# Kernel tuning notes

Hardware: AMD Instinct MI355X
Metric: run time of the kernel (lower is better)

Reference implementation:

```python
import jax, jax.numpy as jnp
import numpy as np
from jax import lax

H, W = 64, 64          # image_shape grid
TOP_K = 3
N_ITER = 50
EPS = 1e-8
NPTS = 3072            # N = M feature points (<= H*W)
SQRT2 = 1.4142135623730951
INV_SQRT3 = 1.0 / 1.7320508075688772


def setup_inputs() -> dict:
    key = jax.random.key(0)
    P = jax.random.uniform(key, (NPTS + 1, NPTS + 1), dtype=jnp.float32)
    K = jnp.array([[500.0, 0.0, 320.0],
                   [0.0, 500.0, 240.0],
                   [0.0, 0.0, 1.0]], dtype=jnp.float32)
    return {"P": P, "K": K}


def _power_iter(Mm, v0):
    # n_iter steps of v <- Mm @ v / ||.||  (differentiable via scan)
    def step(v, _):
        v = Mm @ v
        return v / (jnp.linalg.norm(v) + EPS), None
    v, _ = lax.scan(step, v0, None, length=N_ITER)
    return v


def _det3(M):
    return (M[0, 0] * (M[1, 1] * M[2, 2] - M[1, 2] * M[2, 1])
            - M[0, 1] * (M[1, 0] * M[2, 2] - M[1, 2] * M[2, 0])
            + M[0, 2] * (M[1, 0] * M[2, 1] - M[1, 1] * M[2, 0]))


def _hartley(pts, w):
    # weighted centroid + scale so weighted RMS distance = sqrt(2)
    ws = w.sum() + EPS
    c = (w[:, None] * pts).sum(0) / ws
    pc = pts - c
    md = jnp.sqrt((w * (pc ** 2).sum(-1)).sum() / ws + EPS)
    s = jnp.asarray(SQRT2, pts.dtype) / (md + EPS)
    z = jnp.zeros((), pts.dtype)
    o = jnp.ones((), pts.dtype)
    T = jnp.stack([jnp.stack([s, z, -s * c[0]]),
                   jnp.stack([z, s, -s * c[1]]),
                   jnp.stack([z, z, o])])
    return T, s, c


def _project_E(E):
    # project onto essential manifold: singular values -> [s, s, 0]
    B = E.T @ E
    lam = jnp.trace(B)
    v0 = jnp.full((3,), INV_SQRT3, E.dtype)
    v1 = _power_iter(B, v0)                                   # max eigvec of E^T E
    v3 = _power_iter(lam * jnp.eye(3, dtype=E.dtype) - B, v0)  # min eigvec
    v2 = jnp.cross(v3, v1)
    v2 = v2 / (jnp.linalg.norm(v2) + EPS)
    V = jnp.stack([v1, v2, v3], axis=-1)
    one = jnp.ones((), E.dtype)
    sV = jnp.sign(_det3(V))
    V = V * jnp.stack([one, one, sV])[None, :]
    Ev1 = E @ V[:, 0]
    Ev2 = E @ V[:, 1]
    s1 = jnp.linalg.norm(Ev1)
    s2 = jnp.linalg.norm(Ev2)
    s_avg = (s1 + s2) / 2.0
    u1 = Ev1 / (s1 + EPS)
    u2 = Ev2 / (s2 + EPS)
    u3 = jnp.cross(u1, u2)
    U = jnp.stack([u1, u2, u3], axis=-1)
    sU = jnp.sign(_det3(U))
    U = U * jnp.stack([one, one, sU])[None, :]
    z = jnp.zeros((), E.dtype)
    # U @ diag(s_avg, s_avg, 0) @ V^T, diag folded into column scaling
    return (U * jnp.stack([s_avg, s_avg, z])[None, :]) @ V.T


def reference(P, K):
    N = P.shape[0] - 1
    M = P.shape[1] - 1
    Pc = P[:N, :M]
    # bidirectional top-k + absolute threshold
    tr = lax.top_k(Pc, TOP_K)[0][:, TOP_K - 1]          # (N,) row thresholds
    tc = lax.top_k(Pc.T, TOP_K)[0][:, TOP_K - 1]        # (M,) col thresholds
    mask = (Pc >= tr[:, None]) & (Pc >= tc[None, :]) & (Pc > 0.01)
    weights = Pc * mask.astype(Pc.dtype)
    # grid pixel coords -> normalized camera coords via K^-1
    idx = jnp.arange(H * W, dtype=Pc.dtype)
    pix = jnp.stack([idx % W, jnp.floor(idx / W)], axis=-1)  # (HW, 2)
    K_inv = jnp.linalg.inv(K)
    p1h = jnp.concatenate([pix[:N], jnp.ones((N, 1), Pc.dtype)], axis=-1)
    p2h = jnp.concatenate([pix[:M], jnp.ones((M, 1), Pc.dtype)], axis=-1)
    pts1 = (p1h @ K_inv.T)[:, :2]
    pts2 = (p2h @ K_inv.T)[:, :2]
    w1 = weights.sum(1)
    w2 = weights.sum(0)
    T1, s1, c1 = _hartley(pts1, w1)
    T2, s2, c2 = _hartley(pts2, w2)
    p1 = (pts1 - c1) * s1
    p2 = (pts2 - c2) * s2
    x1, y1 = p1[:, 0], p1[:, 1]
    x2, y2 = p2[:, 0], p2[:, 1]
    on = jnp.ones((N,), Pc.dtype)
    om = jnp.ones((M,), Pc.dtype)
    # (N, M, 9) epipolar design matrix
    A = jnp.stack([x1[:, None] * x2[None, :], x1[:, None] * y2[None, :], x1[:, None] * om[None, :],
                   y1[:, None] * x2[None, :], y1[:, None] * y2[None, :], y1[:, None] * om[None, :],
                   on[:, None] * x2[None, :], on[:, None] * y2[None, :], jnp.ones((N, M), Pc.dtype)],
                  axis=-1)
    A9 = A.reshape(N * M, 9)
    Mmat = (A9 * weights.reshape(-1, 1)).T @ A9            # 9x9 weighted Gram
    # min eigenvector via shifted power iteration
    lam = jnp.trace(Mmat)
    Ms = lam * jnp.eye(9, dtype=Mmat.dtype) - Mmat
    v = _power_iter(Ms, jnp.full((9,), 1.0 / 3.0, Mmat.dtype))
    E_raw = v.reshape(3, 3)
    E = T2.T @ E_raw @ T1                                   # Hartley denormalize
    return _project_E(E)
```

## Files before the change

kernel.cpp:

```cpp
#include <hip/hip_runtime.h>
#include <math.h>

#define NPV 3072
#define LDP 3073
#define EPSF 1e-8f
#define NMOM 52
#define NSEG 64
#define NCHUNK 12
#define NTILE (NSEG * NCHUNK)
#define NMOMBLK 12
#define NPART (NMOMBLK * 4)

#define INS3(v, a, b, c) do { \
    float _m1 = fminf((a), (v)); (a) = fmaxf((a), (v)); \
    float _m2 = fminf((b), _m1); (b) = fmaxf((b), _m1); \
    (c) = fmaxf((c), _m2); } while (0)

#define MRG3(x, y, z, a, b, c) do { \
    INS3((x), a, b, c); INS3((y), a, b, c); INS3((z), a, b, c); } while (0)

#define INSJ(v, j, a, ja, b, jb, c, jc) do { \
    bool _g1 = (v) > (a); \
    bool _g2 = (v) > (b); \
    bool _g3 = (v) > (c); \
    float _nc = _g2 ? (b) : (_g3 ? (v) : (c)); \
    int  _njc = _g2 ? (jb) : (_g3 ? (j) : (jc)); \
    float _nb = _g1 ? (a) : (_g2 ? (v) : (b)); \
    int  _njb = _g1 ? (ja) : (_g2 ? (j) : (jb)); \
    (a) = _g1 ? (v) : (a); \
    (ja) = _g1 ? (j) : (ja); \
    (b) = _nb; (jb) = _njb; \
    (c) = _nc; (jc) = _njc; } while (0)

__device__ __forceinline__ void kinv6(const float* __restrict__ Kmat,
        float& ki0, float& ki1, float& ki2, float& ki3, float& ki4, float& ki5)
{
    float k00 = Kmat[0], k01 = Kmat[1], k02 = Kmat[2];
    float k10 = Kmat[3], k11 = Kmat[4], k12 = Kmat[5];
    float k20 = Kmat[6], k21 = Kmat[7], k22 = Kmat[8];
    float det = k00 * (k11 * k22 - k12 * k21) - k01 * (k10 * k22 - k12 * k20) + k02 * (k10 * k21 - k11 * k20);
    float id = 1.0f / det;
    ki0 = (k11 * k22 - k12 * k21) * id; ki1 = (k02 * k21 - k01 * k22) * id; ki2 = (k01 * k12 - k02 * k11) * id;
    ki3 = (k12 * k20 - k10 * k22) * id; ki4 = (k00 * k22 - k02 * k20) * id; ki5 = (k02 * k10 - k00 * k12) * id;
}

__global__ __launch_bounds__(256) void k_tile(const float* __restrict__ P,
        float4* __restrict__ part, float* __restrict__ rpv, int* __restrict__ rpj)
{
    __shared__ float lds[48][257];
    int t = threadIdx.x;
    int chunk = blockIdx.x % NCHUNK;
    int seg   = blockIdx.x / NCHUNK;
    int j0 = chunk * 256;
    int i0 = seg * 48;
    const float* base = P + (size_t)i0 * LDP + j0 + t;

    float a0 = -1e30f, b0 = -1e30f, c0 = -1e30f;
    float a1 = -1e30f, b1 = -1e30f, c1 = -1e30f;
    float a2 = -1e30f, b2 = -1e30f, c2 = -1e30f;
    float a3 = -1e30f, b3 = -1e30f, c3 = -1e30f;
    float a4 = -1e30f, b4 = -1e30f, c4 = -1e30f;
    float a5 = -1e30f, b5 = -1e30f, c5 = -1e30f;
    float a6 = -1e30f, b6 = -1e30f, c6 = -1e30f;
    float a7 = -1e30f, b7 = -1e30f, c7 = -1e30f;
    #pragma unroll
    for (int r = 0; r < 48; r += 8) {
        float v0 = base[(size_t)(r + 0) * LDP];
        float v1 = base[(size_t)(r + 1) * LDP];
        float v2 = base[(size_t)(r + 2) * LDP];
        float v3 = base[(size_t)(r + 3) * LDP];
        float v4 = base[(size_t)(r + 4) * LDP];
        float v5 = base[(size_t)(r + 5) * LDP];
        float v6 = base[(size_t)(r + 6) * LDP];
        float v7 = base[(size_t)(r + 7) * LDP];
        lds[r + 0][t] = v0;
        lds[r + 1][t] = v1;
        lds[r + 2][t] = v2;
        lds[r + 3][t] = v3;
        lds[r + 4][t] = v4;
        lds[r + 5][t] = v5;
        lds[r + 6][t] = v6;
        lds[r + 7][t] = v7;
        INS3(v0, a0, b0, c0);
        INS3(v1, a1, b1, c1);
        INS3(v2, a2, b2, c2);
        INS3(v3, a3, b3, c3);
        INS3(v4, a4, b4, c4);
        INS3(v5, a5, b5, c5);
        INS3(v6, a6, b6, c6);
        INS3(v7, a7, b7, c7);
    }
    MRG3(a1, b1, c1, a0, b0, c0);
    MRG3(a2, b2, c2, a0, b0, c0);
    MRG3(a3, b3, c3, a0, b0, c0);
    MRG3(a4, b4, c4, a0, b0, c0);
    MRG3(a5, b5, c5, a0, b0, c0);
    MRG3(a6, b6, c6, a0, b0, c0);
    MRG3(a7, b7, c7, a0, b0, c0);
    part[(size_t)seg * NPV + j0 + t] = make_float4(a0, b0, c0, 0.f);

    __syncthreads();

    if (t < 48) {
        float A0 = -1e30f, B0 = -1e30f, C0 = -1e30f; int JA0 = 0, JB0 = 0, JC0 = 0;
        float A1 = -1e30f, B1 = -1e30f, C1 = -1e30f; int JA1 = 0, JB1 = 0, JC1 = 0;
        float A2 = -1e30f, B2 = -1e30f, C2 = -1e30f; int JA2 = 0, JB2 = 0, JC2 = 0;
        float A3 = -1e30f, B3 = -1e30f, C3 = -1e30f; int JA3 = 0, JB3 = 0, JC3 = 0;
        #pragma unroll 8
        for (int s = 0; s < 256; s += 4) {
            float v0 = lds[t][s + 0];
            float v1 = lds[t][s + 1];
            float v2 = lds[t][s + 2];
            float v3 = lds[t][s + 3];
            INSJ(v0, j0 + s + 0, A0, JA0, B0, JB0, C0, JC0);
            INSJ(v1, j0 + s + 1, A1, JA1, B1, JB1, C1, JC1);
            INSJ(v2, j0 + s + 2, A2, JA2, B2, JB2, C2, JC2);
            INSJ(v3, j0 + s + 3, A3, JA3, B3, JB3, C3, JC3);
        }
        INSJ(A1, JA1, A0, JA0, B0, JB0, C0, JC0);
        INSJ(B1, JB1, A0, JA0, B0, JB0, C0, JC0);
        INSJ(C1, JC1, A0, JA0, B0, JB0, C0, JC0);
        INSJ(A2, JA2, A0, JA0, B0, JB0, C0, JC0);
        INSJ(B2, JB2, A0, JA0, B0, JB0, C0, JC0);
        INSJ(C2, JC2, A0, JA0, B0, JB0, C0, JC0);
        INSJ(A3, JA3, A0, JA0, B0, JB0, C0, JC0);
        INSJ(B3, JB3, A0, JA0, B0, JB0, C0, JC0);
        INSJ(C3, JC3, A0, JA0, B0, JB0, C0, JC0);
        int i = i0 + t;
        rpv[(chunk * 3 + 0) * NPV + i] = A0;
        rpv[(chunk * 3 + 1) * NPV + i] = B0;
        rpv[(chunk * 3 + 2) * NPV + i] = C0;
        rpj[(chunk * 3 + 0) * NPV + i] = JA0;
        rpj[(chunk * 3 + 1) * NPV + i] = JB0;
        rpj[(chunk * 3 + 2) * NPV + i] = JC0;
    }
}

__global__ __launch_bounds__(256) void k_colmerge(const float4* __restrict__ part,
        float* __restrict__ tc, int* __restrict__ ticket)
{
    if (blockIdx.x == 0 && threadIdx.x == 0) *ticket = 0;
    int sub = threadIdx.x & 15;
    int j = blockIdx.x * 16 + (threadIdx.x >> 4);
    float4 buf[NSEG / 16];
    #pragma unroll
    for (int k = 0; k < NSEG / 16; ++k)
        buf[k] = part[(size_t)(sub + (k << 4)) * NPV + j];
    float a = -1e30f, b = -1e30f, c = -1e30f;
    #pragma unroll
    for (int k = 0; k < NSEG / 16; ++k) MRG3(buf[k].x, buf[k].y, buf[k].z, a, b, c);
    #pragma unroll
    for (int off = 1; off < 16; off <<= 1) {
        float xa = __shfl_xor(a, off);
        float xb = __shfl_xor(b, off);
        float xc = __shfl_xor(c, off);
        MRG3(xa, xb, xc, a, b, c);
    }
    if (sub == 0) tc[j] = c;
}

__device__ __forceinline__ void acc_pair(float* m, float w, float xs1, float ys1,
                                         float xs2, float ys2)
{
    m[0] += w;
    m[1] += w * xs1; m[2] += w * ys1; m[3] += w * (xs1 * xs1 + ys1 * ys1);
    m[4] += w * xs2; m[5] += w * ys2; m[6] += w * (xs2 * xs2 + ys2 * ys2);
    float a[9] = { xs1 * xs2, xs1 * ys2, xs1, ys1 * xs2, ys1 * ys2, ys1, xs2, ys2, 1.f };
    int idx = 7;
    #pragma unroll
    for (int u = 0; u < 9; ++u) {
        float wa = w * a[u];
        #pragma unroll
        for (int v = u; v < 9; ++v) { m[idx] = fmaf(wa, a[v], m[idx]); ++idx; }
    }
}

__device__ __forceinline__ void mm3r(const float* A, const float* B, float* C) {
    #pragma unroll
    for (int r = 0; r < 3; ++r)
        #pragma unroll
        for (int c = 0; c < 3; ++c)
            C[r * 3 + c] = A[r * 3 + 0] * B[0 + c] + A[r * 3 + 1] * B[3 + c] + A[r * 3 + 2] * B[6 + c];
}

__device__ __forceinline__ float det3(const float* M) {
    return M[0] * (M[4] * M[8] - M[5] * M[7])
         - M[1] * (M[3] * M[8] - M[5] * M[6])
         + M[2] * (M[3] * M[7] - M[4] * M[6]);
}

__device__ void ph_tail(const float* __restrict__ Kmat,
        const float* __restrict__ momp, float* __restrict__ out, int t)
{
    __shared__ float sMom[NMOM];
    __shared__ float sM[81], sY[81], sP[81], sT[81];
    __shared__ float sT1[9], sT2[9];

    if (t < NMOM) {
        float s = 0.f;
        #pragma unroll 8
        for (int b = 0; b < NPART; ++b) s += momp[(size_t)b * 64 + t];
        sMom[t] = s;
    }
    __syncthreads();

    float ki0, ki1, ki2, ki3, ki4, ki5;
    kinv6(Kmat, ki0, ki1, ki2, ki3, ki4, ki5);
    float u0x = ki0 * 31.5f + ki1 * 23.5f + ki2;
    float u0y = ki3 * 31.5f + ki4 * 23.5f + ki5;

    float Sw = sMom[0];
    float ws = Sw + EPSF;
    float c1x = sMom[1] / ws, c1y = sMom[2] / ws;
    float c2x = sMom[4] / ws, c2y = sMom[5] / ws;
    float q1 = (sMom[3] - 2.f * (c1x * sMom[1] + c1y * sMom[2]) + (c1x * c1x + c1y * c1y) * Sw) / ws;
    float q2 = (sMom[6] - 2.f * (c2x * sMom[4] + c2y * sMom[5]) + (c2x * c2x + c2y * c2y) * Sw) / ws;
    float md1 = sqrtf(fmaxf(q1, 0.f) + EPSF);
    float md2 = sqrtf(fmaxf(q2, 0.f) + EPSF);
    float s1 = 1.4142135623730951f / (md1 + EPSF);
    float s2 = 1.4142135623730951f / (md2 + EPSF);

    if (t < 81) {
        int r = t / 9, c = t % 9;
        int u = r < c ? r : c, v = r < c ? c : r;
        int idx = 7 + u * 9 - (u * (u + 1)) / 2 + v;
        sM[t] = sMom[idx];
    }
    if (t == 0) {
        sT1[0] = s1; sT1[1] = 0.f; sT1[2] = -s1 * c1x;
        sT1[3] = 0.f; sT1[4] = s1; sT1[5] = -s1 * c1y;
        sT1[6] = 0.f; sT1[7] = 0.f; sT1[8] = 1.f;
        sT2[0] = s2; sT2[1] = 0.f; sT2[2] = -s2 * c2x;
        sT2[3] = 0.f; sT2[4] = s2; sT2[5] = -s2 * c2y;
        sT2[6] = 0.f; sT2[7] = 0.f; sT2[8] = 1.f;
    }
    __syncthreads();

    if (t < 81) {
        int k = t / 9, c = t % 9;
        float s = 0.f;
        #pragma unroll
        for (int l = 0; l < 9; ++l)
            s = fmaf(sM[k * 9 + l], sT1[(c / 3) * 3 + (l / 3)] * sT2[(c % 3) * 3 + (l % 3)], s);
        sY[t] = s;
    }
    __syncthreads();
    if (t < 81) {
        int r = t / 9, c = t % 9;
        float s = 0.f;
        #pragma unroll
        for (int k = 0; k < 9; ++k)
            s = fmaf(sT1[(r / 3) * 3 + (k / 3)] * sT2[(r % 3) * 3 + (k % 3)], sY[k * 9 + c], s);
        sP[t] = s;
    }
    __syncthreads();
    if (t < 81) {
        int r = t / 9, c = t % 9;
        float lam = sP[0] + sP[10] + sP[20] + sP[30] + sP[40] + sP[50] + sP[60] + sP[70] + sP[80];
        float il = 1.f / (lam + 1e-30f);
        sM[t] = ((r == c ? lam : 0.f) - sP[t]) * il;
    }
    __syncthreads();

#define MM81(DST, A, B) \
    if (t < 81) { \
        int _r = t / 9, _c = t % 9; \
        float _s = 0.f; \
        _Pragma("unroll") \
        for (int _k = 0; _k < 9; ++_k) _s = fmaf(A[_r * 9 + _k], B[_k * 9 + _c], _s); \
        DST[t] = _s; \
    } \
    __syncthreads();

    MM81(sY, sM, sM)
    MM81(sP, sY, sY)
    MM81(sT, sP, sP)
    MM81(sP, sT, sT)
    MM81(sT, sP, sP)
    MM81(sM, sT, sP)
    MM81(sT, sM, sY)
#undef MM81

    if (t < 64) {
        float v9[9];
        float nrm = 0.f;
        #pragma unroll
        for (int r = 0; r < 9; ++r) {
            float s = 0.f;
            #pragma unroll
            for (int c = 0; c < 9; ++c) s += sT[r * 9 + c];
            v9[r] = s * (1.f / 3.f);
            nrm += v9[r] * v9[r];
        }
        nrm = sqrtf(nrm) + EPSF;
        #pragma unroll
        for (int r = 0; r < 9; ++r) v9[r] /= nrm;

        float C1x = c1x + u0x, C1y = c1y + u0y;
        float C2x = c2x + u0x, C2y = c2y + u0y;
        float T1f[9] = { s1, 0.f, -s1 * C1x, 0.f, s1, -s1 * C1y, 0.f, 0.f, 1.f };
        float T2t[9] = { s2, 0.f, 0.f, 0.f, s2, 0.f, -s2 * C2x, -s2 * C2y, 1.f };
        float M1[9], Ee[9];
        mm3r(v9, T1f, M1);
        mm3r(T2t, M1, Ee);

        float B[9];
        #pragma unroll
        for (int r = 0; r < 3; ++r)
            #pragma unroll
            for (int c = 0; c < 3; ++c)
                B[r * 3 + c] = Ee[r] * Ee[c] + Ee[3 + r] * Ee[3 + c] + Ee[6 + r] * Ee[6 + c];
        float lam3 = B[0] + B[4] + B[8];
        float il3 = 1.f / (lam3 + 1e-30f);

        int parity = t & 1;
        float P1[9];
        #pragma unroll
        for (int k = 0; k < 9; ++k) {
            float d = (k == 0 || k == 4 || k == 8) ? lam3 : 0.f;
            P1[k] = (parity ? (d - B[k]) : B[k]) * il3;
        }
        float P2[9], P4[9], P8[9], P16[9], P32[9], R1[9], P50[9];
        mm3r(P1, P1, P2);
        mm3r(P2, P2, P4);
        mm3r(P4, P4, P8);
        mm3r(P8, P8, P16);
        mm3r(P16, P16, P32);
        mm3r(P32, P16, R1);
        mm3r(R1, P2, P50);
        float vx = (P50[0] + P50[1] + P50[2]) * 0.57735026918962584f;
        float vy = (P50[3] + P50[4] + P50[5]) * 0.57735026918962584f;
        float vz = (P50[6] + P50[7] + P50[8]) * 0.57735026918962584f;
        float vn = sqrtf(vx * vx + vy * vy + vz * vz) + EPSF;
        vx /= vn; vy /= vn; vz /= vn;

        float v3x = __shfl(vx, 1), v3y = __shfl(vy, 1), v3z = __shfl(vz, 1);

        if (t == 0) {
            float v1[3] = { vx, vy, vz };
            float v3[3] = { v3x, v3y, v3z };
            float v2[3];
            v2[0] = v3[1] * v1[2] - v3[2] * v1[1];
            v2[1] = v3[2] * v1[0] - v3[0] * v1[2];
            v2[2] = v3[0] * v1[1] - v3[1] * v1[0];
            float n2 = sqrtf(v2[0] * v2[0] + v2[1] * v2[1] + v2[2] * v2[2]) + EPSF;
            v2[0] /= n2; v2[1] /= n2; v2[2] /= n2;
            float V[9];
            #pragma unroll
            for (int r = 0; r < 3; ++r) { V[r * 3 + 0] = v1[r]; V[r * 3 + 1] = v2[r]; V[r * 3 + 2] = v3[r]; }
            float dV = det3(V);
            float sV = (dV > 0.f) ? 1.f : ((dV < 0.f) ? -1.f : 0.f);
            V[2] *= sV; V[5] *= sV; V[8] *= sV;
            float Ev1[3], Ev2[3];
            #pragma unroll
            for (int r = 0; r < 3; ++r) {
                Ev1[r] = Ee[r * 3] * V[0] + Ee[r * 3 + 1] * V[3] + Ee[r * 3 + 2] * V[6];
                Ev2[r] = Ee[r * 3] * V[1] + Ee[r * 3 + 1] * V[4] + Ee[r * 3 + 2] * V[7];
            }
            float s1n = sqrtf(Ev1[0] * Ev1[0] + Ev1[1] * Ev1[1] + Ev1[2] * Ev1[2]);
            float s2n = sqrtf(Ev2[0] * Ev2[0] + Ev2[1] * Ev2[1] + Ev2[2] * Ev2[2]);
            float s_avg = (s1n + s2n) * 0.5f;
            float u1[3], u2[3];
            #pragma unroll
            for (int r = 0; r < 3; ++r) { u1[r] = Ev1[r] / (s1n + EPSF); u2[r] = Ev2[r] / (s2n + EPSF); }
            #pragma unroll
            for (int r = 0; r < 3; ++r)
                #pragma unroll
                for (int c = 0; c < 3; ++c)
                    out[r * 3 + c] = s_avg * (u1[r] * V[c * 3 + 0] + u2[r] * V[c * 3 + 1]);
        }
    }
}

__global__ __launch_bounds__(256) void k_rowmom(const float* __restrict__ Kmat,
        const float* __restrict__ tc, const float* __restrict__ rpv,
        const int* __restrict__ rpj, float* __restrict__ momp,
        int* __restrict__ ticket, float* __restrict__ out)
{
    __shared__ int slast;
    int t = threadIdx.x;
    int i = blockIdx.x * 256 + t;

    float A = -1e30f, B = -1e30f, C = -1e30f;
    int JA = 0, JB = 0, JC = 0;
    #pragma unroll
    for (int ch = 0; ch < NCHUNK; ++ch) {
        #pragma unroll
        for (int k = 0; k < 3; ++k) {
            float v = rpv[(size_t)(ch * 3 + k) * NPV + i];
            int   j = rpj[(size_t)(ch * 3 + k) * NPV + i];
            INSJ(v, j, A, JA, B, JB, C, JC);
        }
    }

    float ki0, ki1, ki2, ki3, ki4, ki5;
    kinv6(Kmat, ki0, ki1, ki2, ki3, ki4, ki5);
    float m[NMOM];
    #pragma unroll
    for (int k = 0; k < NMOM; ++k) m[k] = 0.f;
    float xg = (float)(i & 63) - 31.5f, yg = (float)(i >> 6) - 23.5f;
    float xs1 = ki0 * xg + ki1 * yg;
    float ys1 = ki3 * xg + ki4 * yg;
#define ACCJ(V, J) do { \
    if ((V) > 0.01f && (V) >= tc[J]) { \
        float _xg = (float)((J) & 63) - 31.5f, _yg = (float)((J) >> 6) - 23.5f; \
        float xs2 = ki0 * _xg + ki1 * _yg; \
        float ys2 = ki3 * _xg + ki4 * _yg; \
        acc_pair(m, (V), xs1, ys1, xs2, ys2); \
    } } while (0)
    ACCJ(A, JA);
    ACCJ(B, JB);
    ACCJ(C, JC);
#undef ACCJ

    #pragma unroll
    for (int k = 0; k < NMOM; ++k) {
        #pragma unroll
        for (int off = 32; off; off >>= 1) m[k] += __shfl_xor(m[k], off);
    }
    int lane = t & 63, wid = t >> 6;
    if (lane == 0) {
        float* dst = momp + (size_t)(blockIdx.x * 4 + wid) * 64;
        #pragma unroll
        for (int k = 0; k < NMOM; ++k) dst[k] = m[k];
    }

    __threadfence();
    __syncthreads();
    if (t == 0) slast = (atomicAdd(ticket, 1) == NMOMBLK - 1) ? 1 : 0;
    __syncthreads();
    if (!slast) return;
    __threadfence();
    ph_tail(Kmat, momp, out, t);
}

extern "C" void kernel_launch(void* const* d_in, const int* in_sizes, int n_in,
                              void* d_out, int out_size, void* d_ws, size_t ws_size,
                              hipStream_t stream)
{
    const float* P = (const float*)d_in[0];
    const float* K = (const float*)d_in[1];
    float* out = (float*)d_out;

    float* fws   = (float*)d_ws;
    float* tc    = fws;
    float* rpv   = tc + NPV;
    int*   rpj   = (int*)(rpv + 36 * NPV);
    float* momp  = (float*)(rpj + 36 * NPV);
    int*   ticket = (int*)(momp + NPART * 64);
    float4* part = (float4*)(ticket + 16);

    k_tile    <<<NTILE, 256, 0, stream>>>(P, part, rpv, rpj);
    k_colmerge<<<NPV / 16, 256, 0, stream>>>(part, tc, ticket);
    k_rowmom  <<<NMOMBLK, 256, 0, stream>>>(K, tc, rpv, rpj, momp, ticket, out);
}
```

Before: 44.52 us.

## Restructure top-k scan: column-wise indexed top-3 plus separate row-threshold pass

The pipeline changes from three kernels to two. The column scan now tracks row indices alongside the column top-3, so the per-row top-3 index pass through LDS goes away. A separate set of blocks in the same launch computes each row's third-largest value by reading rows directly. The merge kernel then combines the column partials with their indices, accumulates moments across 192 blocks, and runs the tail in the last block. This drops one launch and the LDS transpose, but P is now read twice (once by columns, once by rows), and the column scan uses more registers for its index tracking.

Result: slower. 48.38 us (+8.7%).

```diff
diff --git a/kernel.cpp b/kernel.cpp
--- a/kernel.cpp
+++ b/kernel.cpp
@@ -6,10 +6,11 @@
 #define EPSF 1e-8f
 #define NMOM 52
 #define NSEG 64
+#define SEGROWS 48
 #define NCHUNK 12
-#define NTILE (NSEG * NCHUNK)
-#define NMOMBLK 12
-#define NPART (NMOMBLK * 4)
+#define NCOLBLK (NSEG * NCHUNK)
+#define NROWBLK 768
+#define NMRG 192
 
 #define INS3(v, a, b, c) do { \
     float _m1 = fminf((a), (v)); (a) = fmaxf((a), (v)); \
@@ -19,18 +20,18 @@
 #define MRG3(x, y, z, a, b, c) do { \
     INS3((x), a, b, c); INS3((y), a, b, c); INS3((z), a, b, c); } while (0)
 
-#define INSJ(v, j, a, ja, b, jb, c, jc) do { \
+#define INSJ(v, i, a, ia, b, ib, c, ic) do { \
     bool _g1 = (v) > (a); \
     bool _g2 = (v) > (b); \
     bool _g3 = (v) > (c); \
     float _nc = _g2 ? (b) : (_g3 ? (v) : (c)); \
-    int  _njc = _g2 ? (jb) : (_g3 ? (j) : (jc)); \
+    int  _nic = _g2 ? (ib) : (_g3 ? (i) : (ic)); \
     float _nb = _g1 ? (a) : (_g2 ? (v) : (b)); \
-    int  _njb = _g1 ? (ja) : (_g2 ? (j) : (jb)); \
+    int  _nib = _g1 ? (ia) : (_g2 ? (i) : (ib)); \
     (a) = _g1 ? (v) : (a); \
-    (ja) = _g1 ? (j) : (ja); \
-    (b) = _nb; (jb) = _njb; \
-    (c) = _nc; (jc) = _njc; } while (0)
+    (ia) = _g1 ? (i) : (ia); \
+    (b) = _nb; (ib) = _nib; \
+    (c) = _nc; (ic) = _nic; } while (0)
 
 __device__ __forceinline__ void kinv6(const float* __restrict__ Kmat,
         float& ki0, float& ki1, float& ki2, float& ki3, float& ki4, float& ki5)
@@ -44,119 +45,93 @@
     ki3 = (k12 * k20 - k10 * k22) * id; ki4 = (k00 * k22 - k02 * k20) * id; ki5 = (k02 * k10 - k00 * k12) * id;
 }
 
-__global__ __launch_bounds__(256) void k_tile(const float* __restrict__ P,
-        float4* __restrict__ part, float* __restrict__ rpv, int* __restrict__ rpj)
-{
-    __shared__ float lds[48][257];
+__global__ __launch_bounds__(256) void k_scan(const float* __restrict__ P,
+        float* __restrict__ tr, float4* __restrict__ partv, int4* __restrict__ parti,
+        int* __restrict__ ticket)
+{
     int t = threadIdx.x;
-    int chunk = blockIdx.x % NCHUNK;
-    int seg   = blockIdx.x / NCHUNK;
-    int j0 = chunk * 256;
-    int i0 = seg * 48;
-    const float* base = P + (size_t)i0 * LDP + j0 + t;
-
-    float a0 = -1e30f, b0 = -1e30f, c0 = -1e30f;
-    float a1 = -1e30f, b1 = -1e30f, c1 = -1e30f;
-    float a2 = -1e30f, b2 = -1e30f, c2 = -1e30f;
-    float a3 = -1e30f, b3 = -1e30f, c3 = -1e30f;
-    float a4 = -1e30f, b4 = -1e30f, c4 = -1e30f;
-    float a5 = -1e30f, b5 = -1e30f, c5 = -1e30f;
-    float a6 = -1e30f, b6 = -1e30f, c6 = -1e30f;
-    float a7 = -1e30f, b7 = -1e30f, c7 = -1e30f;
-    #pragma unroll
-    for (int r = 0; r < 48; r += 8) {
-        float v0 = base[(size_t)(r + 0) * LDP];
-        float v1 = base[(size_t)(r + 1) * LDP];
-        float v2 = base[(size_t)(r + 2) * LDP];
-        float v3 = base[(size_t)(r + 3) * LDP];
-        float v4 = base[(size_t)(r + 4) * LDP];
-        float v5 = base[(size_t)(r + 5) * LDP];
-        float v6 = base[(size_t)(r + 6) * LDP];
-        float v7 = base[(size_t)(r + 7) * LDP];
-        lds[r + 0][t] = v0;
-        lds[r + 1][t] = v1;
-        lds[r + 2][t] = v2;
-        lds[r + 3][t] = v3;
-        lds[r + 4][t] = v4;
-        lds[r + 5][t] = v5;
-        lds[r + 6][t] = v6;
-        lds[r + 7][t] = v7;
-        INS3(v0, a0, b0, c0);
-        INS3(v1, a1, b1, c1);
-        INS3(v2, a2, b2, c2);
-        INS3(v3, a3, b3, c3);
-        INS3(v4, a4, b4, c4);
-        INS3(v5, a5, b5, c5);
-        INS3(v6, a6, b6, c6);
-        INS3(v7, a7, b7, c7);
-    }
-    MRG3(a1, b1, c1, a0, b0, c0);
-    MRG3(a2, b2, c2, a0, b0, c0);
-    MRG3(a3, b3, c3, a0, b0, c0);
-    MRG3(a4, b4, c4, a0, b0, c0);
-    MRG3(a5, b5, c5, a0, b0, c0);
-    MRG3(a6, b6, c6, a0, b0, c0);
-    MRG3(a7, b7, c7, a0, b0, c0);
-    part[(size_t)seg * NPV + j0 + t] = make_float4(a0, b0, c0, 0.f);
-
-    __syncthreads();
-
-    if (t < 48) {
-        float A0 = -1e30f, B0 = -1e30f, C0 = -1e30f; int JA0 = 0, JB0 = 0, JC0 = 0;
-        float A1 = -1e30f, B1 = -1e30f, C1 = -1e30f; int JA1 = 0, JB1 = 0, JC1 = 0;
-        float A2 = -1e30f, B2 = -1e30f, C2 = -1e30f; int JA2 = 0, JB2 = 0, JC2 = 0;
-        float A3 = -1e30f, B3 = -1e30f, C3 = -1e30f; int JA3 = 0, JB3 = 0, JC3 = 0;
-        #pragma unroll 8
-        for (int s = 0; s < 256; s += 4) {
-            float v0 = lds[t][s + 0];
-            float v1 = lds[t][s + 1];
-            float v2 = lds[t][s + 2];
-            float v3 = lds[t][s + 3];
-            INSJ(v0, j0 + s + 0, A0, JA0, B0, JB0, C0, JC0);
-            INSJ(v1, j0 + s + 1, A1, JA1, B1, JB1, C1, JC1);
-            INSJ(v2, j0 + s + 2, A2, JA2, B2, JB2, C2, JC2);
-            INSJ(v3, j0 + s + 3, A3, JA3, B3, JB3, C3, JC3);
-        }
-        INSJ(A1, JA1, A0, JA0, B0, JB0, C0, JC0);
-        INSJ(B1, JB1, A0, JA0, B0, JB0, C0, JC0);
-        INSJ(C1, JC1, A0, JA0, B0, JB0, C0, JC0);
-        INSJ(A2, JA2, A0, JA0, B0, JB0, C0, JC0);
-        INSJ(B2, JB2, A0, JA0, B0, JB0, C0, JC0);
-        INSJ(C2, JC2, A0, JA0, B0, JB0, C0, JC0);
-        INSJ(A3, JA3, A0, JA0, B0, JB0, C0, JC0);
-        INSJ(B3, JB3, A0, JA0, B0, JB0, C0, JC0);
-        INSJ(C3, JC3, A0, JA0, B0, JB0, C0, JC0);
-        int i = i0 + t;
-        rpv[(chunk * 3 + 0) * NPV + i] = A0;
-        rpv[(chunk * 3 + 1) * NPV + i] = B0;
-        rpv[(chunk * 3 + 2) * NPV + i] = C0;
-        rpj[(chunk * 3 + 0) * NPV + i] = JA0;
-        rpj[(chunk * 3 + 1) * NPV + i] = JB0;
-        rpj[(chunk * 3 + 2) * NPV + i] = JC0;
-    }
-}
-
-__global__ __launch_bounds__(256) void k_colmerge(const float4* __restrict__ part,
-        float* __restrict__ tc, int* __restrict__ ticket)
-{
-    if (blockIdx.x == 0 && threadIdx.x == 0) *ticket = 0;
-    int sub = threadIdx.x & 15;
-    int j = blockIdx.x * 16 + (threadIdx.x >> 4);
-    float4 buf[NSEG / 16];
-    #pragma unroll
-    for (int k = 0; k < NSEG / 16; ++k)
-        buf[k] = part[(size_t)(sub + (k << 4)) * NPV + j];
-    float a = -1e30f, b = -1e30f, c = -1e30f;
-    #pragma unroll
-    for (int k = 0; k < NSEG / 16; ++k) MRG3(buf[k].x, buf[k].y, buf[k].z, a, b, c);
-    #pragma unroll
-    for (int off = 1; off < 16; off <<= 1) {
-        float xa = __shfl_xor(a, off);
-        float xb = __shfl_xor(b, off);
-        float xc = __shfl_xor(c, off);
-        MRG3(xa, xb, xc, a, b, c);
-    }
-    if (sub == 0) tc[j] = c;
+    if (blockIdx.x == 0 && t == 0) *ticket = 0;
+
+    if (blockIdx.x < NCOLBLK) {
+        int g = blockIdx.x;
+        int j = (g % NCHUNK) * 256 + t;
+        int i0 = (g / NCHUNK) * SEGROWS;
+        const float* base = P + (size_t)i0 * LDP + j;
+        float A0 = -1e30f, B0 = -1e30f, C0 = -1e30f; int IA0 = 0, IB0 = 0, IC0 = 0;
+        float A1 = -1e30f, B1 = -1e30f, C1 = -1e30f; int IA1 = 0, IB1 = 0, IC1 = 0;
+        float A2 = -1e30f, B2 = -1e30f, C2 = -1e30f; int IA2 = 0, IB2 = 0, IC2 = 0;
+        float A3 = -1e30f, B3 = -1e30f, C3 = -1e30f; int IA3 = 0, IB3 = 0, IC3 = 0;
+        float A4 = -1e30f, B4 = -1e30f, C4 = -1e30f; int IA4 = 0, IB4 = 0, IC4 = 0;
+        float A5 = -1e30f, B5 = -1e30f, C5 = -1e30f; int IA5 = 0, IB5 = 0, IC5 = 0;
+        float A6 = -1e30f, B6 = -1e30f, C6 = -1e30f; int IA6 = 0, IB6 = 0, IC6 = 0;
+        float A7 = -1e30f, B7 = -1e30f, C7 = -1e30f; int IA7 = 0, IB7 = 0, IC7 = 0;
+        #pragma unroll
+        for (int r = 0; r < SEGROWS; r += 8) {
+            float v0 = base[(size_t)(r + 0) * LDP];
+            float v1 = base[(size_t)(r + 1) * LDP];
+            float v2 = base[(size_t)(r + 2) * LDP];
+            float v3 = base[(size_t)(r + 3) * LDP];
+            float v4 = base[(size_t)(r + 4) * LDP];
+            float v5 = base[(size_t)(r + 5) * LDP];
+            float v6 = base[(size_t)(r + 6) * LDP];
+            float v7 = base[(size_t)(r + 7) * LDP];
+            int ib = i0 + r;
+            INSJ(v0, ib + 0, A0, IA0, B0, IB0, C0, IC0);
+            INSJ(v1, ib + 1, A1, IA1, B1, IB1, C1, IC1);
+            INSJ(v2, ib + 2, A2, IA2, B2, IB2, C2, IC2);
+            INSJ(v3, ib + 3, A3, IA3, B3, IB3, C3, IC3);
+            INSJ(v4, ib + 4, A4, IA4, B4, IB4, C4, IC4);
+            INSJ(v5, ib + 5, A5, IA5, B5, IB5, C5, IC5);
+            INSJ(v6, ib + 6, A6, IA6, B6, IB6, C6, IC6);
+            INSJ(v7, ib + 7, A7, IA7, B7, IB7, C7, IC7);
+        }
+#define MRGJ(x, ix, y, iy, z, iz) do { \
+        INSJ(x, ix, A0, IA0, B0, IB0, C0, IC0); \
+        INSJ(y, iy, A0, IA0, B0, IB0, C0, IC0); \
+        INSJ(z, iz, A0, IA0, B0, IB0, C0, IC0); } while (0)
+        MRGJ(A1, IA1, B1, IB1, C1, IC1);
+        MRGJ(A2, IA2, B2, IB2, C2, IC2);
+        MRGJ(A3, IA3, B3, IB3, C3, IC3);
+        MRGJ(A4, IA4, B4, IB4, C4, IC4);
+        MRGJ(A5, IA5, B5, IB5, C5, IC5);
+        MRGJ(A6, IA6, B6, IB6, C6, IC6);
+        MRGJ(A7, IA7, B7, IB7, C7, IC7);
+#undef MRGJ
+        size_t o = (size_t)(g / NCHUNK) * NPV + j;
+        partv[o] = make_float4(A0, B0, C0, 0.f);
+        parti[o] = make_int4(IA0, IB0, IC0, 0);
+    } else {
+        int g = blockIdx.x - NCOLBLK;
+        int lane = t & 63;
+        int i = g * 4 + (t >> 6);
+        const float* row = P + (size_t)i * LDP;
+        float a0 = -1e30f, b0 = -1e30f, c0 = -1e30f;
+        float a1 = -1e30f, b1 = -1e30f, c1 = -1e30f;
+        float a2 = -1e30f, b2 = -1e30f, c2 = -1e30f;
+        float a3 = -1e30f, b3 = -1e30f, c3 = -1e30f;
+        #pragma unroll
+        for (int r = 0; r < 48; r += 4) {
+            float v0 = row[(r + 0) * 64 + lane];
+            float v1 = row[(r + 1) * 64 + lane];
+            float v2 = row[(r + 2) * 64 + lane];
+            float v3 = row[(r + 3) * 64 + lane];
+            INS3(v0, a0, b0, c0);
+            INS3(v1, a1, b1, c1);
+            INS3(v2, a2, b2, c2);
+            INS3(v3, a3, b3, c3);
+        }
+        MRG3(a1, b1, c1, a0, b0, c0);
+        MRG3(a2, b2, c2, a0, b0, c0);
+        MRG3(a3, b3, c3, a0, b0, c0);
+        #pragma unroll
+        for (int off = 1; off < 64; off <<= 1) {
+            float xa = __shfl_xor(a0, off);
+            float xb = __shfl_xor(b0, off);
+            float xc = __shfl_xor(c0, off);
+            MRG3(xa, xb, xc, a0, b0, c0);
+        }
+        if (lane == 0) tr[i] = c0;
+    }
 }
 
 __device__ __forceinline__ void acc_pair(float* m, float w, float xs1, float ys1,
@@ -199,7 +174,7 @@
     if (t < NMOM) {
         float s = 0.f;
         #pragma unroll 8
-        for (int b = 0; b < NPART; ++b) s += momp[(size_t)b * 64 + t];
+        for (int b = 0; b < NMRG; ++b) s += momp[(size_t)b * 64 + t];
         sMom[t] = s;
     }
     __syncthreads();
@@ -372,62 +347,75 @@
     }
 }
 
-__global__ __launch_bounds__(256) void k_rowmom(const float* __restrict__ Kmat,
-        const float* __restrict__ tc, const float* __restrict__ rpv,
-        const int* __restrict__ rpj, float* __restrict__ momp,
+__global__ __launch_bounds__(256) void k_merge_mom_tail(const float* __restrict__ Kmat,
+        const float* __restrict__ tr, const float4* __restrict__ partv,
+        const int4* __restrict__ parti, float* __restrict__ momp,
         int* __restrict__ ticket, float* __restrict__ out)
 {
+    __shared__ float sRed[4][NMOM];
     __shared__ int slast;
     int t = threadIdx.x;
-    int i = blockIdx.x * 256 + t;
+    int sub = t & 15;
+    int j = blockIdx.x * 16 + (t >> 4);
 
     float A = -1e30f, B = -1e30f, C = -1e30f;
-    int JA = 0, JB = 0, JC = 0;
-    #pragma unroll
-    for (int ch = 0; ch < NCHUNK; ++ch) {
-        #pragma unroll
-        for (int k = 0; k < 3; ++k) {
-            float v = rpv[(size_t)(ch * 3 + k) * NPV + i];
-            int   j = rpj[(size_t)(ch * 3 + k) * NPV + i];
-            INSJ(v, j, A, JA, B, JB, C, JC);
-        }
-    }
-
-    float ki0, ki1, ki2, ki3, ki4, ki5;
-    kinv6(Kmat, ki0, ki1, ki2, ki3, ki4, ki5);
+    int IA = 0, IB = 0, IC = 0;
+    #pragma unroll
+    for (int k = 0; k < 4; ++k) {
+        size_t o = (size_t)(sub + (k << 4)) * NPV + j;
+        float4 v = partv[o];
+        int4  iv = parti[o];
+        INSJ(v.x, iv.x, A, IA, B, IB, C, IC);
+        INSJ(v.y, iv.y, A, IA, B, IB, C, IC);
+        INSJ(v.z, iv.z, A, IA, B, IB, C, IC);
+    }
+    #pragma unroll
+    for (int off = 1; off < 16; off <<= 1) {
+        float xa = __shfl_xor(A, off), xb = __shfl_xor(B, off), xc = __shfl_xor(C, off);
+        int   ya = __shfl_xor(IA, off), yb = __shfl_xor(IB, off), yc = __shfl_xor(IC, off);
+        INSJ(xa, ya, A, IA, B, IB, C, IC);
+        INSJ(xb, yb, A, IA, B, IB, C, IC);
+        INSJ(xc, yc, A, IA, B, IB, C, IC);
+    }
+
     float m[NMOM];
     #pragma unroll
     for (int k = 0; k < NMOM; ++k) m[k] = 0.f;
-    float xg = (float)(i & 63) - 31.5f, yg = (float)(i >> 6) - 23.5f;
-    float xs1 = ki0 * xg + ki1 * yg;
-    float ys1 = ki3 * xg + ki4 * yg;
-#define ACCJ(V, J) do { \
-    if ((V) > 0.01f && (V) >= tc[J]) { \
-        float _xg = (float)((J) & 63) - 31.5f, _yg = (float)((J) >> 6) - 23.5f; \
-        float xs2 = ki0 * _xg + ki1 * _yg; \
-        float ys2 = ki3 * _xg + ki4 * _yg; \
-        acc_pair(m, (V), xs1, ys1, xs2, ys2); \
-    } } while (0)
-    ACCJ(A, JA);
-    ACCJ(B, JB);
-    ACCJ(C, JC);
-#undef ACCJ
-
+    if (sub == 0) {
+        float ki0, ki1, ki2, ki3, ki4, ki5;
+        kinv6(Kmat, ki0, ki1, ki2, ki3, ki4, ki5);
+        float xj = (float)(j & 63) - 31.5f, yj = (float)(j >> 6) - 23.5f;
+        float xs2 = ki0 * xj + ki1 * yj;
+        float ys2 = ki3 * xj + ki4 * yj;
+#define ACCI(V, I) do { \
+        if ((V) > 0.01f && (V) >= tr[I]) { \
+            float _xg = (float)((I) & 63) - 31.5f, _yg = (float)((I) >> 6) - 23.5f; \
+            float xs1 = ki0 * _xg + ki1 * _yg; \
+            float ys1 = ki3 * _xg + ki4 * _yg; \
+            acc_pair(m, (V), xs1, ys1, xs2, ys2); \
+        } } while (0)
+        ACCI(A, IA);
+        ACCI(B, IB);
+        ACCI(C, IC);
+#undef ACCI
+    }
     #pragma unroll
     for (int k = 0; k < NMOM; ++k) {
-        #pragma unroll
-        for (int off = 32; off; off >>= 1) m[k] += __shfl_xor(m[k], off);
+        m[k] += __shfl_xor(m[k], 16);
+        m[k] += __shfl_xor(m[k], 32);
     }
     int lane = t & 63, wid = t >> 6;
     if (lane == 0) {
-        float* dst = momp + (size_t)(blockIdx.x * 4 + wid) * 64;
-        #pragma unroll
-        for (int k = 0; k < NMOM; ++k) dst[k] = m[k];
-    }
+        #pragma unroll
+        for (int k = 0; k < NMOM; ++k) sRed[wid][k] = m[k];
+    }
+    __syncthreads();
+    if (t < NMOM)
+        momp[(size_t)blockIdx.x * 64 + t] = sRed[0][t] + sRed[1][t] + sRed[2][t] + sRed[3][t];
 
     __threadfence();
     __syncthreads();
-    if (t == 0) slast = (atomicAdd(ticket, 1) == NMOMBLK - 1) ? 1 : 0;
+    if (t == 0) slast = (atomicAdd(ticket, 1) == NMRG - 1) ? 1 : 0;
     __syncthreads();
     if (!slast) return;
     __threadfence();
@@ -442,15 +430,13 @@
     const float* K = (const float*)d_in[1];
     float* out = (float*)d_out;
 
-    float* fws   = (float*)d_ws;
-    float* tc    = fws;
-    float* rpv   = tc + NPV;
-    int*   rpj   = (int*)(rpv + 36 * NPV);
-    float* momp  = (float*)(rpj + 36 * NPV);
-    int*   ticket = (int*)(momp + NPART * 64);
-    float4* part = (float4*)(ticket + 16);
-
-    k_tile    <<<NTILE, 256, 0, stream>>>(P, part, rpv, rpj);
-    k_colmerge<<<NPV / 16, 256, 0, stream>>>(part, tc, ticket);
-    k_rowmom  <<<NMOMBLK, 256, 0, stream>>>(K, tc, rpv, rpj, momp, ticket, out);
-}
+    float* fws    = (float*)d_ws;
+    float* tr     = fws;
+    float* momp   = tr + NPV;
+    int*   ticket = (int*)(momp + NMRG * 64);
+    float4* partv = (float4*)(ticket + 16);
+    int4*   parti = (int4*)(partv + (size_t)NSEG * NPV);
+
+    k_scan<<<NCOLBLK + NROWBLK, 256, 0, stream>>>(P, tr, partv, parti, ticket);
+    k_merge_mom_tail<<<NMRG, 256, 0, stream>>>(K, tr, partv, parti, momp, ticket, out);
+}
```
